# Performance work log

Hardware: AMD Instinct MI355X
Metric: run time of the kernel (lower is better)

The kernel has to match this reference:

```python
import jax, jax.numpy as jnp
import numpy as np

B, T, D = 2, 2048, 1024
HEADS = 16
MEM = 512
HEAD_DIM = D // HEADS


def setup_inputs() -> dict:
    key = jax.random.key(0)
    k1, k2, k3, k4, k5 = jax.random.split(key, 5)
    x = jax.random.normal(k1, (B, T, D), dtype=jnp.float32)
    w_qkv = jax.random.normal(k2, (3 * D, D), dtype=jnp.float32) * (1.0 / np.sqrt(D))
    w_out = jax.random.normal(k3, (D, D), dtype=jnp.float32) * (1.0 / np.sqrt(D))
    b_out = jax.random.normal(k4, (D,), dtype=jnp.float32) * 0.01
    memory = jax.random.normal(k5, (MEM, D), dtype=jnp.float32)
    return {"x": x, "w_qkv": w_qkv, "w_out": w_out, "b_out": b_out, "memory": memory}


def reference(x, w_qkv, w_out, b_out, memory):
    b, t, d = x.shape
    h, hd = HEADS, HEAD_DIM
    scale = hd ** -0.5
    # QKV projection: [B,T,3D]
    qkv = jnp.einsum('btd,ed->bte', x, w_qkv)
    q, k, v = jnp.split(qkv, 3, axis=-1)
    # [B,H,T,hd]
    q = q.reshape(b, t, h, hd).transpose(0, 2, 1, 3)
    k = k.reshape(b, t, h, hd).transpose(0, 2, 1, 3)
    v = v.reshape(b, t, h, hd).transpose(0, 2, 1, 3)
    # memory K/V: [B,H,MEM,hd] (broadcast over batch)
    mem = memory.reshape(1, MEM, h, hd).transpose(0, 2, 1, 3)
    mem = jnp.broadcast_to(mem, (b, h, MEM, hd))
    k = jnp.concatenate([mem, k], axis=2)
    v = jnp.concatenate([mem, v], axis=2)
    # attention: scores [B,H,T,MEM+T]
    scores = jnp.einsum('bhqd,bhkd->bhqk', q, k) * scale
    weights = jax.nn.softmax(scores, axis=-1)
    out = jnp.einsum('bhqk,bhkd->bhqd', weights, v)
    out = out.transpose(0, 2, 1, 3).reshape(b, t, d)
    return jnp.einsum('btd,ed->bte', out, w_out) + b_out
```

## Files before the change

kernel.cpp:

```cpp
#include <hip/hip_runtime.h>
#include <hip/hip_bf16.h>
#include <stdint.h>

#define B_   2
#define T_   2048
#define D_   1024
#define H_   16
#define HD_  64
#define MEM_ 512
#define KV_  (MEM_ + T_)
#define NIT_ (KV_ / 64)

using bf16 = __bf16;
typedef __bf16 bf16x8 __attribute__((ext_vector_type(8)));
typedef float  f32x4  __attribute__((ext_vector_type(4)));
typedef short  s16x4  __attribute__((ext_vector_type(4)));

__device__ __forceinline__ f32x4 mfma16(bf16x8 a, bf16x8 b, f32x4 c) {
  return __builtin_amdgcn_mfma_f32_16x16x32_bf16(a, b, c, 0, 0, 0);
}
__device__ __forceinline__ f32x4 mfma16k16(s16x4 a, s16x4 b, f32x4 c) {
  return __builtin_amdgcn_mfma_f32_16x16x16bf16_1k(a, b, c, 0, 0, 0);
}

__device__ __forceinline__ void gll16(const void* g, void* l) {
  __builtin_amdgcn_global_load_lds(
      (const __attribute__((address_space(1))) unsigned int*)g,
      (__attribute__((address_space(3))) unsigned int*)l, 16, 0, 0);
}

__device__ __forceinline__ unsigned short bf16_bits(float f) {
  bf16 h = (bf16)f;
  return __builtin_bit_cast(unsigned short, h);
}

__device__ __forceinline__ ushort4 pack4(f32x4 v) {
  ushort4 p;
  p.x = bf16_bits(v[0]); p.y = bf16_bits(v[1]);
  p.z = bf16_bits(v[2]); p.w = bf16_bits(v[3]);
  return p;
}

__global__ void conv_bf16(const float* __restrict__ s, bf16* __restrict__ d) {
  size_t i = ((size_t)blockIdx.x * 256 + threadIdx.x) * 8;
  f32x4 a = *(const f32x4*)(s + i);
  f32x4 b = *(const f32x4*)(s + i + 4);
  bf16x8 r;
  r[0] = (bf16)a[0]; r[1] = (bf16)a[1]; r[2] = (bf16)a[2]; r[3] = (bf16)a[3];
  r[4] = (bf16)b[0]; r[5] = (bf16)b[1]; r[6] = (bf16)b[2]; r[7] = (bf16)b[3];
  *(bf16x8*)(d + i) = r;
}

__global__ void fill_mem(const float* __restrict__ memory,
                         bf16* __restrict__ mem_k, bf16* __restrict__ mem_vt) {
  int idx = blockIdx.x * 256 + threadIdx.x;
  int m = idx >> 10, d = idx & 1023;
  int hh = d >> 6, hd = d & 63;
  bf16 v = (bf16)memory[idx];
  mem_k[((size_t)hh * MEM_ + m) * HD_ + hd] = v;
  mem_vt[(size_t)d * MEM_ + m] = v;
}

template <int EPI, bool APLANE>
__global__ __launch_bounds__(256) void gemm_bt(
    const bf16* __restrict__ A, const bf16* __restrict__ W,
    const float* __restrict__ bias,
    bf16* __restrict__ q_ws, bf16* __restrict__ k_ws, bf16* __restrict__ vt_ws,
    float* __restrict__ Cout, int K) {
  __shared__ __align__(16) bf16 Als[128 * 32];
  __shared__ __align__(16) bf16 Bls[128 * 32];
  char* AB = (char*)Als;
  char* BB = (char*)Bls;
  const int m0 = blockIdx.y * 128;
  const int n0 = blockIdx.x * 128;
  const int tid = threadIdx.x;
  const int w = tid >> 6;
  const int lane = tid & 63;
  const int lx = lane & 15;
  const int quad = lane >> 4;
  const int amb = (w & 1) * 64;
  const int bnb = (w >> 1) * 64;
  const int r0 = tid >> 2;
  const int cs = (tid & 3) ^ ((tid >> 3) & 3);
  const int rsw = (lx >> 1) & 3;

  f32x4 acc[4][4];
#pragma unroll
  for (int i = 0; i < 4; i++)
#pragma unroll
    for (int j = 0; j < 4; j++) acc[i][j] = (f32x4){0.f, 0.f, 0.f, 0.f};

  for (int k0 = 0; k0 < K; k0 += 32) {
    const bf16 *pa0, *pa1;
    if constexpr (APLANE) {
      int c0 = k0 + cs * 8, hh = c0 >> 6, hd = c0 & 63;
      int mA = m0 + r0, mB = mA + 64;
      pa0 = A + ((size_t)((mA >> 11) * H_ + hh) * T_ + (mA & 2047)) * HD_ + hd;
      pa1 = A + ((size_t)((mB >> 11) * H_ + hh) * T_ + (mB & 2047)) * HD_ + hd;
    } else {
      pa0 = A + (size_t)(m0 + r0) * K + k0 + cs * 8;
      pa1 = pa0 + (size_t)64 * K;
    }
    const bf16* pb0 = W + (size_t)(n0 + r0) * K + k0 + cs * 8;
    const bf16* pb1 = pb0 + (size_t)64 * K;

    __syncthreads();
    gll16(pa0, AB + tid * 16);
    gll16(pa1, AB + tid * 16 + 4096);
    gll16(pb0, BB + tid * 16);
    gll16(pb1, BB + tid * 16 + 4096);
    __syncthreads();

    bf16x8 af[4], bfr[4];
#pragma unroll
    for (int mt = 0; mt < 4; mt++)
      af[mt] = *(const bf16x8*)(AB + (size_t)(amb + mt * 16 + lx) * 64 +
                                ((quad ^ rsw) * 16));
#pragma unroll
    for (int nt = 0; nt < 4; nt++)
      bfr[nt] = *(const bf16x8*)(BB + (size_t)(bnb + nt * 16 + lx) * 64 +
                                 ((quad ^ rsw) * 16));
#pragma unroll
    for (int mt = 0; mt < 4; mt++)
#pragma unroll
      for (int nt = 0; nt < 4; nt++)
        acc[mt][nt] = mfma16(af[mt], bfr[nt], acc[mt][nt]);
  }

  if (EPI == 0) {
#pragma unroll
    for (int mt = 0; mt < 4; mt++) {
      int mbase = m0 + amb + mt * 16 + quad * 4;
      int b = mbase >> 11;
      int t = mbase & 2047;
#pragma unroll
      for (int nt = 0; nt < 4; nt++) {
        int col = n0 + bnb + nt * 16 + lx;
        int which = col >> 10;
        int d = col & 1023;
        int hh = d >> 6, hdi = d & 63;
        int bh = b * H_ + hh;
        if (which == 0) {
#pragma unroll
          for (int r = 0; r < 4; r++)
            q_ws[((size_t)bh * T_ + t + r) * HD_ + hdi] = (bf16)acc[mt][nt][r];
        } else if (which == 1) {
#pragma unroll
          for (int r = 0; r < 4; r++)
            k_ws[((size_t)bh * T_ + t + r) * HD_ + hdi] = (bf16)acc[mt][nt][r];
        } else {
          *(ushort4*)&vt_ws[((size_t)bh * HD_ + hdi) * T_ + t] =
              pack4(acc[mt][nt]);
        }
      }
    }
  } else {
#pragma unroll
    for (int nt = 0; nt < 4; nt++) {
      int col = n0 + bnb + nt * 16 + lx;
      float bias_f = bias[col];
#pragma unroll
      for (int mt = 0; mt < 4; mt++) {
        int mbase = m0 + amb + mt * 16 + quad * 4;
#pragma unroll
        for (int r = 0; r < 4; r++)
          Cout[(size_t)(mbase + r) * D_ + col] = acc[mt][nt][r] + bias_f;
      }
    }
  }
}

__global__ __launch_bounds__(256, 2) void attn_kernel(
    bf16* __restrict__ q_ws, const bf16* __restrict__ k_ws,
    const bf16* __restrict__ vt_ws, const bf16* __restrict__ mem_k,
    const bf16* __restrict__ mem_vt) {
  __shared__ __align__(16) bf16 Kls[64 * 64];
  __shared__ __align__(16) bf16 Vls[64 * 64];
  char* KB = (char*)Kls;
  char* VB = (char*)Vls;
  const int tid = threadIdx.x;
  const int w = tid >> 6;
  const int lane = tid & 63;
  const int lx = lane & 15;
  const int quad = lane >> 4;
  const int bh = blockIdx.x & 31;
  const int qt = blockIdx.x >> 5;
  const int q0 = qt * 128 + w * 32;
  const int h = bh & 15;

  const int srow1 = tid >> 3;
  const int sc1 = (tid & 7) ^ (srow1 & 7);

  bf16* qbase = q_ws + ((size_t)bh * T_ + q0) * HD_;

  const float QSCALE = 0.125f * 1.44269504089f;
  bf16x8 qf[2][2];
#pragma unroll
  for (int qg = 0; qg < 2; qg++)
#pragma unroll
    for (int hf = 0; hf < 2; hf++) {
      bf16x8 v = *(const bf16x8*)(qbase + (size_t)(qg * 16 + lx) * HD_ +
                                  hf * 32 + quad * 8);
#pragma unroll
      for (int i = 0; i < 8; i++)
        v[i] = (bf16)((float)v[i] * QSCALE);
      qf[qg][hf] = v;
    }

  const bf16* kpl = k_ws + (size_t)bh * T_ * HD_;
  const bf16* vpl = vt_ws + (size_t)bh * HD_ * T_;
  const bf16* mkp = mem_k + (size_t)h * MEM_ * HD_;
  const bf16* mvp = mem_vt + (size_t)h * HD_ * MEM_;

  f32x4 o[4][2];
#pragma unroll
  for (int mt = 0; mt < 4; mt++)
#pragma unroll
    for (int qg = 0; qg < 2; qg++) o[mt][qg] = (f32x4){0.f, 0.f, 0.f, 0.f};
  float lsum[2] = {0.f, 0.f};

  for (int it = 0; it < NIT_; it++) {
    const int kv0 = it * 64;
    const bf16 *kp1, *kp2, *vp1, *vp2;
    if (kv0 < MEM_) {
      kp1 = mkp + (size_t)(kv0 + srow1) * HD_ + sc1 * 8;
      kp2 = kp1 + (size_t)32 * HD_;
      vp1 = mvp + (size_t)srow1 * MEM_ + kv0 + sc1 * 8;
      vp2 = vp1 + (size_t)32 * MEM_;
    } else {
      const int t0 = kv0 - MEM_;
      kp1 = kpl + (size_t)(t0 + srow1) * HD_ + sc1 * 8;
      kp2 = kp1 + (size_t)32 * HD_;
      vp1 = vpl + (size_t)srow1 * T_ + t0 + sc1 * 8;
      vp2 = vp1 + (size_t)32 * T_;
    }
    __syncthreads();
    gll16(kp1, KB + tid * 16);
    gll16(kp2, KB + tid * 16 + 4096);
    gll16(vp1, VB + tid * 16);
    gll16(vp2, VB + tid * 16 + 4096);
    __syncthreads();

    const int sw = (lx & 7) << 4;
    f32x4 s[4][2];
#pragma unroll
    for (int g = 0; g < 4; g++) {
      const char* kb = KB + (size_t)(g * 16 + lx) * 128;
      bf16x8 ka0 = *(const bf16x8*)(kb + ((quad * 16) ^ sw));
      bf16x8 ka1 = *(const bf16x8*)(kb + ((64 + quad * 16) ^ sw));
#pragma unroll
      for (int qg = 0; qg < 2; qg++) {
        s[g][qg] = (f32x4){0.f, 0.f, 0.f, 0.f};
        s[g][qg] = mfma16(ka0, qf[qg][0], s[g][qg]);
        s[g][qg] = mfma16(ka1, qf[qg][1], s[g][qg]);
      }
    }

    s16x4 pb[2][4];
#pragma unroll
    for (int qg = 0; qg < 2; qg++) {
      float ps = 0.f;
#pragma unroll
      for (int g = 0; g < 4; g++) {
#pragma unroll
        for (int r = 0; r < 4; r++) {
          float p = __builtin_amdgcn_exp2f(s[g][qg][r]);
          ps += p;
          pb[qg][g][r] = (short)bf16_bits(p);
        }
      }
      lsum[qg] += ps;
    }

#pragma unroll
    for (int mt = 0; mt < 4; mt++) {
      const char* vb = VB + (size_t)(mt * 16 + lx) * 128;
#pragma unroll
      for (int kk = 0; kk < 4; kk++) {
        s16x4 va = *(const s16x4*)(vb + ((kk * 32 + quad * 8) ^ sw));
#pragma unroll
        for (int qg = 0; qg < 2; qg++)
          o[mt][qg] = mfma16k16(va, pb[qg][kk], o[mt][qg]);
      }
    }
  }

  float inv[2];
#pragma unroll
  for (int qg = 0; qg < 2; qg++) {
    float s2 = lsum[qg];
    s2 += __shfl_xor(s2, 16);
    s2 += __shfl_xor(s2, 32);
    inv[qg] = 1.f / s2;
  }

#pragma unroll
  for (int qg = 0; qg < 2; qg++) {
#pragma unroll
    for (int mt = 0; mt < 4; mt++) {
      f32x4 ov;
#pragma unroll
      for (int r = 0; r < 4; r++) ov[r] = o[mt][qg][r] * inv[qg];
      *(ushort4*)(qbase + (size_t)(qg * 16 + lx) * HD_ + mt * 16 + quad * 4)
          = pack4(ov);
    }
  }
}

extern "C" void kernel_launch(void* const* d_in, const int* in_sizes, int n_in,
                              void* d_out, int out_size, void* d_ws,
                              size_t ws_size, hipStream_t stream) {
  const float* x      = (const float*)d_in[0];
  const float* w_qkv  = (const float*)d_in[1];
  const float* w_out  = (const float*)d_in[2];
  const float* b_out  = (const float*)d_in[3];
  const float* memory = (const float*)d_in[4];

  char* ws = (char*)d_ws;
  bf16* q_ws   = (bf16*)(ws);
  bf16* k_ws   = (bf16*)(ws + (8u << 20));
  bf16* vt_ws  = (bf16*)(ws + (16u << 20));
  bf16* mem_k  = (bf16*)(ws + (24u << 20));
  bf16* mem_vt = (bf16*)(ws + (25u << 20));
  float* out = (float*)d_out;

  char* outc = (char*)d_out;
  bf16* xb  = (bf16*)(outc);
  bf16* wqb = (bf16*)(outc + (8u << 20));
  bf16* wob = (bf16*)(ws + (8u << 20));

  conv_bf16<<<dim3(2048), dim3(256), 0, stream>>>(x, xb);
  conv_bf16<<<dim3(1536), dim3(256), 0, stream>>>(w_qkv, wqb);
  fill_mem<<<dim3(2048), dim3(256), 0, stream>>>(memory, mem_k, mem_vt);
  gemm_bt<0, false><<<dim3(24, 32), dim3(256), 0, stream>>>(
      xb, wqb, nullptr, q_ws, k_ws, vt_ws, nullptr, 1024);
  attn_kernel<<<dim3(512), dim3(256), 0, stream>>>(
      q_ws, k_ws, vt_ws, mem_k, mem_vt);
  conv_bf16<<<dim3(512), dim3(256), 0, stream>>>(w_out, wob);
  gemm_bt<1, true><<<dim3(8, 32), dim3(256), 0, stream>>>(
      q_ws, wob, b_out, nullptr, nullptr, nullptr, out, 1024);
}
```

Measured before the change: 222.3 us.

## Double-buffer attention KV loads, widen GEMM K-step, fuse prep kernels

Merges the x/w_qkv conversion and the memory fill into a single prep launch, with vectorized memory reads. The GEMM now steps K by 64 per stage, and the output projection uses a 64-wide N tile so it launches more blocks. The attention kernel double-buffers K/V tiles in LDS, issuing the next tile's async loads before computing on the current one, and raises wave priority around the MFMA phases. The intent is to hide load latency and cut launch overhead, at the cost of doubled attention LDS (which may affect occupancy at 2 blocks/CU) and more register pressure in the GEMM.

```diff
diff --git a/kernel.cpp b/kernel.cpp
--- a/kernel.cpp
+++ b/kernel.cpp
@@ -41,90 +41,122 @@
   return p;
 }
 
+__device__ __forceinline__ bf16x8 cvt8(f32x4 a, f32x4 b) {
+  bf16x8 r;
+  r[0] = (bf16)a[0]; r[1] = (bf16)a[1]; r[2] = (bf16)a[2]; r[3] = (bf16)a[3];
+  r[4] = (bf16)b[0]; r[5] = (bf16)b[1]; r[6] = (bf16)b[2]; r[7] = (bf16)b[3];
+  return r;
+}
+
+__global__ void prep(const float* __restrict__ x, const float* __restrict__ wq,
+                     const float* __restrict__ memory,
+                     bf16* __restrict__ xb, bf16* __restrict__ wqb,
+                     bf16* __restrict__ mem_k, bf16* __restrict__ mem_vt) {
+  int blk = blockIdx.x;
+  if (blk < 3584) {
+    const float* s = (blk < 2048) ? x : wq;
+    bf16* d = (blk < 2048) ? xb : wqb;
+    size_t i = ((size_t)(blk < 2048 ? blk : blk - 2048) * 256 + threadIdx.x) * 8;
+    f32x4 a = *(const f32x4*)(s + i);
+    f32x4 b = *(const f32x4*)(s + i + 4);
+    *(bf16x8*)(d + i) = cvt8(a, b);
+  } else {
+    int idx8 = ((blk - 3584) * 256 + threadIdx.x) * 8;
+    int m = idx8 >> 10, d0 = idx8 & 1023;
+    int hh = d0 >> 6, hd0 = d0 & 63;
+    f32x4 a = *(const f32x4*)(memory + idx8);
+    f32x4 b = *(const f32x4*)(memory + idx8 + 4);
+    bf16x8 r = cvt8(a, b);
+    *(bf16x8*)&mem_k[((size_t)hh * MEM_ + m) * HD_ + hd0] = r;
+#pragma unroll
+    for (int j = 0; j < 8; j++)
+      mem_vt[(size_t)(d0 + j) * MEM_ + m] = r[j];
+  }
+}
+
 __global__ void conv_bf16(const float* __restrict__ s, bf16* __restrict__ d) {
   size_t i = ((size_t)blockIdx.x * 256 + threadIdx.x) * 8;
   f32x4 a = *(const f32x4*)(s + i);
   f32x4 b = *(const f32x4*)(s + i + 4);
-  bf16x8 r;
-  r[0] = (bf16)a[0]; r[1] = (bf16)a[1]; r[2] = (bf16)a[2]; r[3] = (bf16)a[3];
-  r[4] = (bf16)b[0]; r[5] = (bf16)b[1]; r[6] = (bf16)b[2]; r[7] = (bf16)b[3];
-  *(bf16x8*)(d + i) = r;
-}
-
-__global__ void fill_mem(const float* __restrict__ memory,
-                         bf16* __restrict__ mem_k, bf16* __restrict__ mem_vt) {
-  int idx = blockIdx.x * 256 + threadIdx.x;
-  int m = idx >> 10, d = idx & 1023;
-  int hh = d >> 6, hd = d & 63;
-  bf16 v = (bf16)memory[idx];
-  mem_k[((size_t)hh * MEM_ + m) * HD_ + hd] = v;
-  mem_vt[(size_t)d * MEM_ + m] = v;
-}
-
-template <int EPI, bool APLANE>
+  *(bf16x8*)(d + i) = cvt8(a, b);
+}
+
+template <int EPI, bool APLANE, int NTILE>
 __global__ __launch_bounds__(256) void gemm_bt(
     const bf16* __restrict__ A, const bf16* __restrict__ W,
     const float* __restrict__ bias,
     bf16* __restrict__ q_ws, bf16* __restrict__ k_ws, bf16* __restrict__ vt_ws,
     float* __restrict__ Cout, int K) {
-  __shared__ __align__(16) bf16 Als[128 * 32];
-  __shared__ __align__(16) bf16 Bls[128 * 32];
+  constexpr int NF = NTILE / 32;
+  constexpr int NB = NTILE / 32;
+  __shared__ __align__(16) bf16 Als[128 * 64];
+  __shared__ __align__(16) bf16 Bls[NTILE * 64];
   char* AB = (char*)Als;
   char* BB = (char*)Bls;
   const int m0 = blockIdx.y * 128;
-  const int n0 = blockIdx.x * 128;
+  const int n0 = blockIdx.x * NTILE;
   const int tid = threadIdx.x;
   const int w = tid >> 6;
   const int lane = tid & 63;
   const int lx = lane & 15;
   const int quad = lane >> 4;
   const int amb = (w & 1) * 64;
-  const int bnb = (w >> 1) * 64;
-  const int r0 = tid >> 2;
-  const int cs = (tid & 3) ^ ((tid >> 3) & 3);
-  const int rsw = (lx >> 1) & 3;
-
-  f32x4 acc[4][4];
+  const int bnb = (w >> 1) * (NTILE / 2);
+  const int srow = tid >> 3;
+  const int cs = (tid & 7) ^ (srow & 7);
+
+  f32x4 acc[4][NF];
 #pragma unroll
   for (int i = 0; i < 4; i++)
 #pragma unroll
-    for (int j = 0; j < 4; j++) acc[i][j] = (f32x4){0.f, 0.f, 0.f, 0.f};
-
-  for (int k0 = 0; k0 < K; k0 += 32) {
-    const bf16 *pa0, *pa1;
-    if constexpr (APLANE) {
-      int c0 = k0 + cs * 8, hh = c0 >> 6, hd = c0 & 63;
-      int mA = m0 + r0, mB = mA + 64;
-      pa0 = A + ((size_t)((mA >> 11) * H_ + hh) * T_ + (mA & 2047)) * HD_ + hd;
-      pa1 = A + ((size_t)((mB >> 11) * H_ + hh) * T_ + (mB & 2047)) * HD_ + hd;
-    } else {
-      pa0 = A + (size_t)(m0 + r0) * K + k0 + cs * 8;
-      pa1 = pa0 + (size_t)64 * K;
-    }
-    const bf16* pb0 = W + (size_t)(n0 + r0) * K + k0 + cs * 8;
-    const bf16* pb1 = pb0 + (size_t)64 * K;
+    for (int j = 0; j < NF; j++) acc[i][j] = (f32x4){0.f, 0.f, 0.f, 0.f};
+
+  for (int k0 = 0; k0 < K; k0 += 64) {
+    const bf16* pa[4];
+#pragma unroll
+    for (int g = 0; g < 4; g++) {
+      int r = srow + 32 * g;
+      if constexpr (APLANE) {
+        int hh = k0 >> 6, hd = cs * 8;
+        int mA = m0 + r;
+        pa[g] = A + ((size_t)((mA >> 11) * H_ + hh) * T_ + (mA & 2047)) * HD_ + hd;
+      } else {
+        pa[g] = A + (size_t)(m0 + r) * K + k0 + cs * 8;
+      }
+    }
+    const bf16* pb[NB];
+#pragma unroll
+    for (int g = 0; g < NB; g++)
+      pb[g] = W + (size_t)(n0 + srow + 32 * g) * K + k0 + cs * 8;
 
     __syncthreads();
-    gll16(pa0, AB + tid * 16);
-    gll16(pa1, AB + tid * 16 + 4096);
-    gll16(pb0, BB + tid * 16);
-    gll16(pb1, BB + tid * 16 + 4096);
+#pragma unroll
+    for (int g = 0; g < 4; g++) gll16(pa[g], AB + g * 4096 + tid * 16);
+#pragma unroll
+    for (int g = 0; g < NB; g++) gll16(pb[g], BB + g * 4096 + tid * 16);
     __syncthreads();
 
-    bf16x8 af[4], bfr[4];
+    bf16x8 af[4][2], bfr[NF][2];
+    const int rk = (lx & 7) << 4;
 #pragma unroll
     for (int mt = 0; mt < 4; mt++)
-      af[mt] = *(const bf16x8*)(AB + (size_t)(amb + mt * 16 + lx) * 64 +
-                                ((quad ^ rsw) * 16));
-#pragma unroll
-    for (int nt = 0; nt < 4; nt++)
-      bfr[nt] = *(const bf16x8*)(BB + (size_t)(bnb + nt * 16 + lx) * 64 +
-                                 ((quad ^ rsw) * 16));
-#pragma unroll
-    for (int mt = 0; mt < 4; mt++)
-#pragma unroll
-      for (int nt = 0; nt < 4; nt++)
-        acc[mt][nt] = mfma16(af[mt], bfr[nt], acc[mt][nt]);
+#pragma unroll
+      for (int kh = 0; kh < 2; kh++)
+        af[mt][kh] = *(const bf16x8*)(AB + (size_t)(amb + mt * 16 + lx) * 128 +
+                                      ((quad * 16 + kh * 64) ^ rk));
+#pragma unroll
+    for (int nt = 0; nt < NF; nt++)
+#pragma unroll
+      for (int kh = 0; kh < 2; kh++)
+        bfr[nt][kh] = *(const bf16x8*)(BB + (size_t)(bnb + nt * 16 + lx) * 128 +
+                                       ((quad * 16 + kh * 64) ^ rk));
+#pragma unroll
+    for (int kh = 0; kh < 2; kh++)
+#pragma unroll
+      for (int mt = 0; mt < 4; mt++)
+#pragma unroll
+        for (int nt = 0; nt < NF; nt++)
+          acc[mt][nt] = mfma16(af[mt][kh], bfr[nt][kh], acc[mt][nt]);
   }
 
   if (EPI == 0) {
@@ -134,7 +166,7 @@
       int b = mbase >> 11;
       int t = mbase & 2047;
 #pragma unroll
-      for (int nt = 0; nt < 4; nt++) {
+      for (int nt = 0; nt < NF; nt++) {
         int col = n0 + bnb + nt * 16 + lx;
         int which = col >> 10;
         int d = col & 1023;
@@ -156,7 +188,7 @@
     }
   } else {
 #pragma unroll
-    for (int nt = 0; nt < 4; nt++) {
+    for (int nt = 0; nt < NF; nt++) {
       int col = n0 + bnb + nt * 16 + lx;
       float bias_f = bias[col];
 #pragma unroll
@@ -174,8 +206,8 @@
     bf16* __restrict__ q_ws, const bf16* __restrict__ k_ws,
     const bf16* __restrict__ vt_ws, const bf16* __restrict__ mem_k,
     const bf16* __restrict__ mem_vt) {
-  __shared__ __align__(16) bf16 Kls[64 * 64];
-  __shared__ __align__(16) bf16 Vls[64 * 64];
+  __shared__ __align__(16) bf16 Kls[2 * 64 * 64];
+  __shared__ __align__(16) bf16 Vls[2 * 64 * 64];
   char* KB = (char*)Kls;
   char* VB = (char*)Vls;
   const int tid = threadIdx.x;
@@ -193,34 +225,13 @@
 
   bf16* qbase = q_ws + ((size_t)bh * T_ + q0) * HD_;
 
-  const float QSCALE = 0.125f * 1.44269504089f;
-  bf16x8 qf[2][2];
-#pragma unroll
-  for (int qg = 0; qg < 2; qg++)
-#pragma unroll
-    for (int hf = 0; hf < 2; hf++) {
-      bf16x8 v = *(const bf16x8*)(qbase + (size_t)(qg * 16 + lx) * HD_ +
-                                  hf * 32 + quad * 8);
-#pragma unroll
-      for (int i = 0; i < 8; i++)
-        v[i] = (bf16)((float)v[i] * QSCALE);
-      qf[qg][hf] = v;
-    }
-
   const bf16* kpl = k_ws + (size_t)bh * T_ * HD_;
   const bf16* vpl = vt_ws + (size_t)bh * HD_ * T_;
   const bf16* mkp = mem_k + (size_t)h * MEM_ * HD_;
   const bf16* mvp = mem_vt + (size_t)h * HD_ * MEM_;
 
-  f32x4 o[4][2];
-#pragma unroll
-  for (int mt = 0; mt < 4; mt++)
-#pragma unroll
-    for (int qg = 0; qg < 2; qg++) o[mt][qg] = (f32x4){0.f, 0.f, 0.f, 0.f};
-  float lsum[2] = {0.f, 0.f};
-
-  for (int it = 0; it < NIT_; it++) {
-    const int kv0 = it * 64;
+  auto stage = [&](int it2, int bi) {
+    const int kv0 = it2 * 64;
     const bf16 *kp1, *kp2, *vp1, *vp2;
     if (kv0 < MEM_) {
       kp1 = mkp + (size_t)(kv0 + srow1) * HD_ + sc1 * 8;
@@ -234,18 +245,56 @@
       vp1 = vpl + (size_t)srow1 * T_ + t0 + sc1 * 8;
       vp2 = vp1 + (size_t)32 * T_;
     }
-    __syncthreads();
-    gll16(kp1, KB + tid * 16);
-    gll16(kp2, KB + tid * 16 + 4096);
-    gll16(vp1, VB + tid * 16);
-    gll16(vp2, VB + tid * 16 + 4096);
-    __syncthreads();
-
+    char* kb = KB + bi * 8192;
+    char* vb = VB + bi * 8192;
+    gll16(kp1, kb + tid * 16);
+    gll16(kp2, kb + tid * 16 + 4096);
+    gll16(vp1, vb + tid * 16);
+    gll16(vp2, vb + tid * 16 + 4096);
+  };
+
+  const float QSCALE = 0.125f * 1.44269504089f;
+  bf16x8 qf[2][2];
+#pragma unroll
+  for (int qg = 0; qg < 2; qg++)
+#pragma unroll
+    for (int hf = 0; hf < 2; hf++) {
+      bf16x8 v = *(const bf16x8*)(qbase + (size_t)(qg * 16 + lx) * HD_ +
+                                  hf * 32 + quad * 8);
+#pragma unroll
+      for (int i = 0; i < 8; i++)
+        v[i] = (bf16)((float)v[i] * QSCALE);
+      qf[qg][hf] = v;
+    }
+
+  f32x4 o[4][2];
+#pragma unroll
+  for (int mt = 0; mt < 4; mt++)
+#pragma unroll
+    for (int qg = 0; qg < 2; qg++) o[mt][qg] = (f32x4){0.f, 0.f, 0.f, 0.f};
+  float lsum[2] = {0.f, 0.f};
+
+  stage(0, 0);
+
+  for (int it = 0; it < NIT_; it++) {
+    const int cur = it & 1;
+    if (it + 1 < NIT_) {
+      stage(it + 1, cur ^ 1);
+      asm volatile("s_waitcnt vmcnt(4)" ::: "memory");
+    } else {
+      asm volatile("s_waitcnt vmcnt(0)" ::: "memory");
+    }
+    __builtin_amdgcn_s_barrier();
+    __builtin_amdgcn_sched_barrier(0);
+
+    const char* KBc = KB + cur * 8192;
+    const char* VBc = VB + cur * 8192;
     const int sw = (lx & 7) << 4;
     f32x4 s[4][2];
+    __builtin_amdgcn_s_setprio(1);
 #pragma unroll
     for (int g = 0; g < 4; g++) {
-      const char* kb = KB + (size_t)(g * 16 + lx) * 128;
+      const char* kb = KBc + (size_t)(g * 16 + lx) * 128;
       bf16x8 ka0 = *(const bf16x8*)(kb + ((quad * 16) ^ sw));
       bf16x8 ka1 = *(const bf16x8*)(kb + ((64 + quad * 16) ^ sw));
 #pragma unroll
@@ -255,6 +304,7 @@
         s[g][qg] = mfma16(ka1, qf[qg][1], s[g][qg]);
       }
     }
+    __builtin_amdgcn_s_setprio(0);
 
     s16x4 pb[2][4];
 #pragma unroll
@@ -272,9 +322,10 @@
       lsum[qg] += ps;
     }
 
+    __builtin_amdgcn_s_setprio(1);
 #pragma unroll
     for (int mt = 0; mt < 4; mt++) {
-      const char* vb = VB + (size_t)(mt * 16 + lx) * 128;
+      const char* vb = VBc + (size_t)(mt * 16 + lx) * 128;
 #pragma unroll
       for (int kk = 0; kk < 4; kk++) {
         s16x4 va = *(const s16x4*)(vb + ((kk * 32 + quad * 8) ^ sw));
@@ -283,6 +334,10 @@
           o[mt][qg] = mfma16k16(va, pb[qg][kk], o[mt][qg]);
       }
     }
+    __builtin_amdgcn_s_setprio(0);
+
+    __builtin_amdgcn_sched_barrier(0);
+    __builtin_amdgcn_s_barrier();
   }
 
   float inv[2];
@@ -329,14 +384,13 @@
   bf16* wqb = (bf16*)(outc + (8u << 20));
   bf16* wob = (bf16*)(ws + (8u << 20));
 
-  conv_bf16<<<dim3(2048), dim3(256), 0, stream>>>(x, xb);
-  conv_bf16<<<dim3(1536), dim3(256), 0, stream>>>(w_qkv, wqb);
-  fill_mem<<<dim3(2048), dim3(256), 0, stream>>>(memory, mem_k, mem_vt);
-  gemm_bt<0, false><<<dim3(24, 32), dim3(256), 0, stream>>>(
+  prep<<<dim3(3840), dim3(256), 0, stream>>>(x, w_qkv, memory,
+                                             xb, wqb, mem_k, mem_vt);
+  gemm_bt<0, false, 128><<<dim3(24, 32), dim3(256), 0, stream>>>(
       xb, wqb, nullptr, q_ws, k_ws, vt_ws, nullptr, 1024);
   attn_kernel<<<dim3(512), dim3(256), 0, stream>>>(
       q_ws, k_ws, vt_ws, mem_k, mem_vt);
   conv_bf16<<<dim3(512), dim3(256), 0, stream>>>(w_out, wob);
-  gemm_bt<1, true><<<dim3(8, 32), dim3(256), 0, stream>>>(
+  gemm_bt<1, true, 64><<<dim3(16, 32), dim3(256), 0, stream>>>(
       q_ws, wob, b_out, nullptr, nullptr, nullptr, out, 1024);
 }
```

Result: faster. 212.8 us (-4.3%).
